# Kernel optimization log

Hardware: AMD Instinct MI355X
Metric: run time of the kernel (lower is better)

## Reference

```python
import jax, jax.numpy as jnp
import numpy as np

NG, K, LEN_KEEP = 128, 32, 32  # n_groups, group_size, int(128*(1-0.75))
ENC_HEADS, DEC_HEADS = 12, 16


def _fps(xyz, init, npoint):
    # iterative farthest point sampling; xyz (B,N,3), init (B,) start indices
    B, N, _ = xyz.shape
    def step(carry, _):
        dmin, far = carry
        c = jnp.take_along_axis(xyz, far[:, None, None], axis=1)  # (B,1,3)
        dmin = jnp.minimum(dmin, jnp.sum((xyz - c) ** 2, -1))
        return (dmin, jnp.argmax(dmin, -1)), far
    _, cents = jax.lax.scan(step, (jnp.full((B, N), 1e10, xyz.dtype), init), None, length=npoint)
    return cents.T  # (B, npoint)


def _knn(xyz, cents, k):
    # squared-distance knn (same ordering as euclidean cdist + topk smallest)
    x2 = jnp.sum(xyz * xyz, -1)          # (B,N)
    c2 = jnp.sum(cents * cents, -1)      # (B,M)
    d = c2[:, :, None] + x2[:, None, :] - 2.0 * jnp.einsum('bmc,bnc->bmn', cents, xyz)
    idx = jax.lax.top_k(-d, k)[1]        # (B,M,k)
    return jax.vmap(lambda p, i: p[i])(xyz, idx)  # (B,M,k,3)


def _bn(x, g, b):
    # train-mode BatchNorm1d over (batch, spatial), channel-last x (BM,k,C)
    m = x.mean((0, 1))
    v = x.var((0, 1))
    return (x - m) * jax.lax.rsqrt(v + 1e-5) * g + b


def _ln(x, g, b):
    m = x.mean(-1, keepdims=True)
    v = ((x - m) ** 2).mean(-1, keepdims=True)
    return (x - m) * jax.lax.rsqrt(v + 1e-5) * g + b


def _layer(x, qw, qb, ow, ob, l1g, l1b, f1w, f1b, f2w, f2b, l2g, l2b, nh):
    # post-norm TransformerEncoderLayer (relu FFN, no dropout = eval mode)
    B, S, D = x.shape
    dh = D // nh
    q, k, v = jnp.split(x @ qw.T + qb, 3, axis=-1)
    q = q.reshape(B, S, nh, dh); k = k.reshape(B, S, nh, dh); v = v.reshape(B, S, nh, dh)
    att = jax.nn.softmax(jnp.einsum('bqhd,bkhd->bhqk', q, k) * (1.0 / float(np.sqrt(dh))), axis=-1)
    o = jnp.einsum('bhqk,bkhd->bqhd', att, v).reshape(B, S, D) @ ow.T + ob
    x = _ln(x + o, l1g, l1b)
    f = jax.nn.relu(x @ f1w.T + f1b) @ f2w.T + f2b
    return _ln(x + f, l2g, l2b)


def _stack(x, qw, qb, ow, ob, l1g, l1b, f1w, f1b, f2w, f2b, l2g, l2b, nh):
    for i in range(qw.shape[0]):
        x = _layer(x, qw[i], qb[i], ow[i], ob[i], l1g[i], l1b[i], f1w[i], f1b[i], f2w[i], f2b[i], l2g[i], l2b[i], nh)
    return x


def _forward(xyz, fps_init, ids_shuffle, cw1, cb1, g1, be1, cw2, cb2, g2, be2, cw3, cb3, g3, be3, pos_w, pos_b, eqw, eqb, eow, eob, el1g, el1b, ef1w, ef1b, ef2w, ef2b, el2g, el2b, dew, deb, mtok, dpw, dpb, dqw, dqb, dow, dob, dl1g, dl1b, df1w, df1b, df2w, df2b, dl2g, dl2b, prw, prb):
    B = xyz.shape[0]
    cent_idx = _fps(xyz, fps_init, NG)
    cxyz = jax.vmap(lambda p, i: p[i])(xyz, cent_idx)      # (B,NG,3)
    gn = _knn(xyz, cxyz, K) - cxyz[:, :, None, :]          # (B,NG,K,3) centered groups
    h = gn.reshape(-1, K, 3)
    h = jax.nn.relu(_bn(h @ cw1.T + cb1, g1, be1))
    h = jax.nn.relu(_bn(h @ cw2.T + cb2, g2, be2))
    h = _bn(h @ cw3.T + cb3, g3, be3)
    tokens = h.max(axis=1).reshape(B, NG, -1)              # (B,NG,768)
    x = tokens + cxyz @ pos_w.T + pos_b
    ids_restore = jnp.argsort(ids_shuffle, axis=1)
    xk = jnp.take_along_axis(x, ids_shuffle[:, :LEN_KEEP, None], axis=1)
    mask = jnp.ones((B, NG), xyz.dtype).at[:, :LEN_KEEP].set(0.0)
    mask = jnp.take_along_axis(mask, ids_restore, axis=1)
    lat = _stack(xk, eqw, eqb, eow, eob, el1g, el1b, ef1w, ef1b, ef2w, ef2b, el2g, el2b, ENC_HEADS)
    y = lat @ dew.T + deb
    mt = jnp.broadcast_to(mtok, (B, NG - LEN_KEEP, mtok.shape[0]))
    y_ = jnp.take_along_axis(jnp.concatenate([y, mt], axis=1), ids_restore[:, :, None], axis=1)
    yd = y_ + cxyz @ dpw.T + dpb
    dec = _stack(yd, dqw, dqb, dow, dob, dl1g, dl1b, df1w, df1b, df2w, df2b, dl2g, dl2b, DEC_HEADS)
    pred = dec @ prw.T + prb                               # (B,NG,K*3)
    target = gn.reshape(B, NG, -1)                         # same FPS seed -> same centroids in loss branch
    l = ((pred - target) ** 2).mean(-1)
    loss = (l * mask).sum() / mask.sum()
    return loss, pred, mask


def setup_inputs():
    ks = iter(jax.random.split(jax.random.key(0), 64))
    def W(*shape):
        return jax.random.normal(next(ks), shape, jnp.float32) * 0.02
    B, N, D, DD, Le, Ld = 32, 8192, 768, 512, 12, 8
    d = {}
    d['xyz'] = jax.random.normal(next(ks), (B, N, 3), jnp.float32)
    d['fps_init'] = jax.random.randint(next(ks), (B,), 0, N)
    d['ids_shuffle'] = jnp.argsort(jax.random.uniform(next(ks), (B, NG)), axis=1)
    d['cw1'], d['cb1'], d['g1'], d['be1'] = W(64, 3), jnp.zeros(64), jnp.ones(64), jnp.zeros(64)
    d['cw2'], d['cb2'], d['g2'], d['be2'] = W(128, 64), jnp.zeros(128), jnp.ones(128), jnp.zeros(128)
    d['cw3'], d['cb3'], d['g3'], d['be3'] = W(D, 128), jnp.zeros(D), jnp.ones(D), jnp.zeros(D)
    d['pos_w'], d['pos_b'] = W(D, 3), jnp.zeros(D)
    d['eqw'], d['eqb'] = W(Le, 3 * D, D), jnp.zeros((Le, 3 * D))
    d['eow'], d['eob'] = W(Le, D, D), jnp.zeros((Le, D))
    d['el1g'], d['el1b'] = jnp.ones((Le, D)), jnp.zeros((Le, D))
    d['ef1w'], d['ef1b'] = W(Le, 4 * D, D), jnp.zeros((Le, 4 * D))
    d['ef2w'], d['ef2b'] = W(Le, D, 4 * D), jnp.zeros((Le, D))
    d['el2g'], d['el2b'] = jnp.ones((Le, D)), jnp.zeros((Le, D))
    d['dew'], d['deb'] = W(DD, D), jnp.zeros(DD)
    d['mtok'] = jnp.zeros(DD)
    d['dpw'], d['dpb'] = W(DD, 3), jnp.zeros(DD)
    d['dqw'], d['dqb'] = W(Ld, 3 * DD, DD), jnp.zeros((Ld, 3 * DD))
    d['dow'], d['dob'] = W(Ld, DD, DD), jnp.zeros((Ld, DD))
    d['dl1g'], d['dl1b'] = jnp.ones((Ld, DD)), jnp.zeros((Ld, DD))
    d['df1w'], d['df1b'] = W(Ld, 4 * DD, DD), jnp.zeros((Ld, 4 * DD))
    d['df2w'], d['df2b'] = W(Ld, DD, 4 * DD), jnp.zeros((Ld, DD))
    d['dl2g'], d['dl2b'] = jnp.ones((Ld, DD)), jnp.zeros((Ld, DD))
    d['prw'], d['prb'] = W(K * 3, DD), jnp.zeros(K * 3)
    return d


def reference(xyz, fps_init, ids_shuffle, cw1, cb1, g1, be1, cw2, cb2, g2, be2, cw3, cb3, g3, be3, pos_w, pos_b, eqw, eqb, eow, eob, el1g, el1b, ef1w, ef1b, ef2w, ef2b, el2g, el2b, dew, deb, mtok, dpw, dpb, dqw, dqb, dow, dob, dl1g, dl1b, df1w, df1b, df2w, df2b, dl2g, dl2b, prw, prb):
    return _forward(xyz, fps_init, ids_shuffle, cw1, cb1, g1, be1, cw2, cb2, g2, be2, cw3, cb3, g3, be3, pos_w, pos_b, eqw, eqb, eow, eob, el1g, el1b, ef1w, ef1b, ef2w, ef2b, el2g, el2b, dew, deb, mtok, dpw, dpb, dqw, dqb, dow, dob, dl1g, dl1b, df1w, df1b, df2w, df2b, dl2g, dl2b, prw, prb)
```

## Files before the change

### kernel.cpp

```cpp
#include <hip/hip_runtime.h>
#include <cmath>

#define BB 32
#define NPTS 8192
#define NG 128
#define KNB 32
#define LK 32
#define DE 768
#define DD 512
#define NLE 12
#define NLD 8

typedef __bf16 bf16x8 __attribute__((ext_vector_type(8)));
typedef float  f32x4  __attribute__((ext_vector_type(4)));
typedef unsigned long long u64;

#define WAITV(N) asm volatile("s_waitcnt vmcnt(" #N ")" ::: "memory")

static __device__ __forceinline__ bf16x8 pack8(float4 a, float4 b) {
    bf16x8 h;
    h[0] = (__bf16)a.x; h[1] = (__bf16)a.y; h[2] = (__bf16)a.z; h[3] = (__bf16)a.w;
    h[4] = (__bf16)b.x; h[5] = (__bf16)b.y; h[6] = (__bf16)b.z; h[7] = (__bf16)b.w;
    return h;
}

static __device__ __forceinline__ void gload16(const __bf16* g, __bf16* l) {
    __builtin_amdgcn_global_load_lds(
        (const __attribute__((address_space(1))) void*)g,
        (__attribute__((address_space(3))) void*)l,
        16, 0, 0);
}

static __device__ __forceinline__ unsigned fkey(float f) {
    unsigned u = __float_as_uint(f);
    return ((int)u < 0) ? ~u : (u | 0x80000000u);
}

__global__ __launch_bounds__(256, 1) void fps_kernel(
    const float* __restrict__ xyz, const int* __restrict__ init,
    float* __restrict__ cxyz)
{
#pragma clang fp contract(off)
    const int b = blockIdx.x;
    const float* P = xyz + (size_t)b * NPTS * 3;
    __shared__ float pxs[NPTS], pys[NPTS], pzs[NPTS];
    __shared__ u64 red[2][4];
    const int tid = threadIdx.x;
    float x[32], y[32], z[32], dmin[32];
    #pragma unroll
    for (int k = 0; k < 32; ++k) {
        int n = tid + (k << 8);
        float xx = P[n * 3 + 0], yy = P[n * 3 + 1], zz = P[n * 3 + 2];
        x[k] = xx; y[k] = yy; z[k] = zz;
        pxs[n] = xx; pys[n] = yy; pzs[n] = zz;
        dmin[k] = 1e10f;
    }
    int far = init[b];
    __syncthreads();
    for (int t = 0; t < NG; ++t) {
        float cx = pxs[far], cy = pys[far], cz = pzs[far];
        if (tid == 0) {
            cxyz[(b * NG + t) * 3 + 0] = cx;
            cxyz[(b * NG + t) * 3 + 1] = cy;
            cxyz[(b * NG + t) * 3 + 2] = cz;
        }
        u64 key = 0ull;
        #pragma unroll
        for (int k = 0; k < 32; ++k) {
            float dx = x[k] - cx, dy = y[k] - cy, dz = z[k] - cz;
            float d = dx * dx + dy * dy + dz * dz;
            float dm = dmin[k];
            if (d < dm) dm = d;
            dmin[k] = dm;
            u64 kk = ((u64)__float_as_uint(dm) << 32) | (unsigned)(8191 - (tid + (k << 8)));
            if (kk > key) key = kk;
        }
        #pragma unroll
        for (int d = 32; d >= 1; d >>= 1) {
            u64 k2 = __shfl_down(key, d);
            if (k2 > key) key = k2;
        }
        if ((tid & 63) == 0) red[t & 1][tid >> 6] = key;
        __syncthreads();
        u64 kb = red[t & 1][0];
        #pragma unroll
        for (int w = 1; w < 4; ++w) {
            u64 k2 = red[t & 1][w];
            if (k2 > kb) kb = k2;
        }
        far = 8191 - (int)(kb & 0xFFFFFFFFu);
    }
}

__global__ __launch_bounds__(256) void knn_kernel(
    const float* __restrict__ xyz, const float* __restrict__ cxyz,
    float* __restrict__ gn)
{
#pragma clang fp contract(off)
    const int bm = blockIdx.x;
    const int b = bm / NG;
    const float* P = xyz + (size_t)b * NPTS * 3;
    __shared__ u64 cand[512];
    __shared__ u64 tmins[4];
    __shared__ int wcnt[4];
    __shared__ int order[KNB];
    const int tid = threadIdx.x;
    const int wv = tid >> 6, lane = tid & 63;
    const float cx = cxyz[bm * 3 + 0], cy = cxyz[bm * 3 + 1], cz = cxyz[bm * 3 + 2];
    const float c2 = cx * cx + cy * cy + cz * cz;
    unsigned fk[32];
    float bestf = 1e31f; int bi = 1 << 30;
    #pragma unroll
    for (int j = 0; j < 32; ++j) {
        int n = tid + (j << 8);
        float x = P[n * 3 + 0], y = P[n * 3 + 1], z = P[n * 3 + 2];
        float x2 = x * x + y * y + z * z;
        float dt = cx * x + cy * y + cz * z;
        float v = (c2 + x2) - 2.0f * dt;
        fk[j] = fkey(v);
        if (v < bestf) { bestf = v; bi = n; }
    }
    u64 mk = ((u64)fkey(bestf) << 32) | (unsigned)bi;
    {
        u64 v = mk;
        #pragma unroll
        for (int k = 2; k <= 64; k <<= 1) {
            #pragma unroll
            for (int j = k >> 1; j > 0; j >>= 1) {
                u64 o = __shfl_xor(v, j);
                bool up = ((lane & k) == 0);
                bool lower = ((lane & j) == 0);
                u64 mn = (v < o) ? v : o;
                u64 mx = (v < o) ? o : v;
                v = (up == lower) ? mn : mx;
            }
        }
        u64 Tw = __shfl(v, 31);
        if (lane == 0) tmins[wv] = Tw;
    }
    __syncthreads();
    u64 T = tmins[0];
    #pragma unroll
    for (int w = 1; w < 4; ++w) { u64 k2 = tmins[w]; if (k2 < T) T = k2; }
    int c = 0;
    #pragma unroll
    for (int j = 0; j < 32; ++j) {
        u64 key = ((u64)fk[j] << 32) | (unsigned)(tid + (j << 8));
        c += (key <= T) ? 1 : 0;
    }
    int s = c;
    #pragma unroll
    for (int d = 1; d < 64; d <<= 1) {
        int t2 = __shfl_up(s, d);
        if (lane >= d) s += t2;
    }
    int excl = s - c;
    if (lane == 63) wcnt[wv] = s;
    __syncthreads();
    int base = 0;
    for (int w = 0; w < wv; ++w) base += wcnt[w];
    int etot = wcnt[0] + wcnt[1] + wcnt[2] + wcnt[3];

    if (etot <= 512) {
        int pos = base + excl;
        #pragma unroll
        for (int j = 0; j < 32; ++j) {
            u64 key = ((u64)fk[j] << 32) | (unsigned)(tid + (j << 8));
            if (key <= T) cand[pos++] = key;
        }
        __syncthreads();
        for (int si = tid; si < etot; si += 256) {
            u64 my = cand[si];
            int r = 0;
            for (int j2 = 0; j2 < etot; ++j2) r += (cand[j2] < my) ? 1 : 0;
            if (r < KNB) order[r] = (int)(my & 0xFFFFFFFFu);
        }
        __syncthreads();
    } else {
        u64 bk = ~0ull;
        #pragma unroll
        for (int j = 0; j < 32; ++j) {
            u64 key = ((u64)fk[j] << 32) | (unsigned)(tid + (j << 8));
            if (key < bk) bk = key;
        }
        for (int r = 0; r < KNB; ++r) {
            u64 kk = bk;
            #pragma unroll
            for (int dd = 32; dd >= 1; dd >>= 1) {
                u64 k2 = __shfl_down(kk, dd);
                if (k2 < kk) kk = k2;
            }
            if (lane == 0) cand[(r & 1) * 4 + wv] = kk;
            __syncthreads();
            u64 kb = cand[(r & 1) * 4 + 0];
            #pragma unroll
            for (int w = 1; w < 4; ++w) { u64 k2 = cand[(r & 1) * 4 + w]; if (k2 < kb) kb = k2; }
            if (tid == 0) order[r] = (int)(kb & 0xFFFFFFFFu);
            if ((int)(kb & 255u) == tid) {
                int sj = (int)((kb & 0xFFFFFFFFu) >> 8);
                #pragma unroll
                for (int j = 0; j < 32; ++j) if (j == sj) fk[j] = 0xFFFFFFFFu;
                bk = ~0ull;
                #pragma unroll
                for (int j = 0; j < 32; ++j) {
                    u64 key = ((u64)fk[j] << 32) | (unsigned)(tid + (j << 8));
                    if (key < bk) bk = key;
                }
            }
            __syncthreads();
        }
    }
    if (tid < KNB) {
        int n = order[tid];
        gn[((size_t)bm * KNB + tid) * 3 + 0] = P[n * 3 + 0] - cx;
        gn[((size_t)bm * KNB + tid) * 3 + 1] = P[n * 3 + 1] - cy;
        gn[((size_t)bm * KNB + tid) * 3 + 2] = P[n * 3 + 2] - cz;
    }
}

__global__ void cvt_bf16_kernel(const float* __restrict__ src, __bf16* __restrict__ dst, int n8)
{
    int i = blockIdx.x * 256 + threadIdx.x;
    if (i >= n8) return;
    const float4* p = (const float4*)(src + (size_t)i * 8);
    *(bf16x8*)(dst + (size_t)i * 8) = pack8(p[0], p[1]);
}

struct CvtTab {
    const float* src[10];
    __bf16* dst[10];
    int cum[11];
};
__global__ void cvt_multi_kernel(CvtTab t)
{
    int i = blockIdx.x * 256 + threadIdx.x;
    if (i >= t.cum[10]) return;
    int seg = 0;
    #pragma unroll
    for (int k = 1; k < 10; ++k) seg += (i >= t.cum[k]) ? 1 : 0;
    int local = i - t.cum[seg];
    const float4* p = (const float4*)(t.src[seg] + (size_t)local * 8);
    *(bf16x8*)(t.dst[seg] + (size_t)local * 8) = pack8(p[0], p[1]);
}

__global__ void embed1_kernel(const float* __restrict__ gn, const float* __restrict__ w,
                              const float* __restrict__ bias, float* __restrict__ h1)
{
    int i = blockIdx.x * 256 + threadIdx.x;
    if (i >= 131072 * 64) return;
    int r = i >> 6, c = i & 63;
    const float* p = gn + (size_t)r * 3;
    h1[i] = p[0] * w[c * 3 + 0] + p[1] * w[c * 3 + 1] + p[2] * w[c * 3 + 2] + bias[c];
}

template <int C>
__global__ __launch_bounds__(256) void colstats_kernel(const float* __restrict__ X,
                                                       double* __restrict__ st, int Mrows)
{
    constexpr int RL = 256 / C;
    const int c = threadIdx.x % C;
    const int rl = threadIdx.x / C;
    double s = 0.0, s2 = 0.0;
    int rows_per_block = (Mrows + gridDim.x - 1) / gridDim.x;
    int r0 = blockIdx.x * rows_per_block;
    int r1 = min(r0 + rows_per_block, Mrows);
    for (int r = r0 + rl; r < r1; r += RL) {
        float v = X[(size_t)r * C + c];
        s += v; s2 += (double)v * v;
    }
    __shared__ double sh[2][256];
    sh[0][threadIdx.x] = s; sh[1][threadIdx.x] = s2;
    __syncthreads();
    if (rl == 0) {
        for (int j = 1; j < RL; ++j) { s += sh[0][j * C + c]; s2 += sh[1][j * C + c]; }
        atomicAdd(&st[c], s);
        atomicAdd(&st[C + c], s2);
    }
}

__global__ void bn_finalize(const double* __restrict__ st, const float* __restrict__ g,
                            const float* __restrict__ be, float* __restrict__ sc,
                            float* __restrict__ shb, int C)
{
    int c = blockIdx.x * 64 + threadIdx.x;
    if (c >= C) return;
    double m = st[c] / 131072.0;
    double var = st[C + c] / 131072.0 - m * m;
    if (var < 0.0) var = 0.0;
    float rs = rsqrtf((float)var + 1e-5f);
    sc[c] = rs * g[c];
    shb[c] = be[c] - (float)m * rs * g[c];
}

__global__ void bn_apply_bf16(const float* __restrict__ x, const float* __restrict__ sc,
                              const float* __restrict__ shb, __bf16* __restrict__ y,
                              int total, int C)
{
    int i = blockIdx.x * 256 + threadIdx.x;
    if (i >= total) return;
    int c = i % C;
    float v = x[i] * sc[c] + shb[c];
    v = fmaxf(v, 0.0f);
    y[i] = (__bf16)v;
}

template <int BM, int WM, int WN, int DEPTH>
__global__ __launch_bounds__(256) void gemm_bf16(
    const __bf16* __restrict__ A, const __bf16* __restrict__ W,
    const float* __restrict__ bias, float* __restrict__ Cf, __bf16* __restrict__ Cb,
    int M, int N, int K, int Kc, int relu)
{
    constexpr int MR = BM / WM / 16;
    constexpr int NR = 128 / WN / 16;
    constexpr int CA = BM * 8 / 256;
    __shared__ __bf16 As[DEPTH][BM * 64];
    __shared__ __bf16 Ws[DEPTH][128 * 64];
    const int tid = threadIdx.x;
    const int lane = tid & 63;
    const int wave = tid >> 6;
    const int wm = wave / WN, wn = wave % WN;
    const int m0 = blockIdx.y * BM, n0 = blockIdx.x * 128;
    const int kb = blockIdx.z * Kc;

    f32x4 acc[MR][NR] = {};

    auto stage = [&](int buf, int kt) {
        #pragma unroll
        for (int j = 0; j < CA; ++j) {
            int cb = j * 256 + (wave << 6);
            int c  = cb + lane;
            int row = c >> 3;
            int kcs = (c & 7) ^ (row & 7);
            gload16(A + (size_t)(m0 + row) * K + kb + kt + kcs * 8, &As[buf][cb * 8]);
        }
        #pragma unroll
        for (int j = 0; j < 4; ++j) {
            int cb = j * 256 + (wave << 6);
            int c  = cb + lane;
            int row = c >> 3;
            int kcs = (c & 7) ^ (row & 7);
            gload16(W + (size_t)(n0 + row) * K + kb + kt + kcs * 8, &Ws[buf][cb * 8]);
        }
    };
    auto compute = [&](int buf) {
        #pragma unroll
        for (int ks = 0; ks < 2; ++ks) {
            bf16x8 af[MR], bfr[NR];
            int kc = ks * 4 + (lane >> 4);
            #pragma unroll
            for (int i = 0; i < MR; ++i) {
                int rowA = wm * (BM / WM) + i * 16 + (lane & 15);
                af[i] = *(bf16x8*)&As[buf][rowA * 64 + ((kc ^ (rowA & 7)) * 8)];
            }
            #pragma unroll
            for (int j = 0; j < NR; ++j) {
                int rowB = wn * (128 / WN) + j * 16 + (lane & 15);
                bfr[j] = *(bf16x8*)&Ws[buf][rowB * 64 + ((kc ^ (rowB & 7)) * 8)];
            }
            #pragma unroll
            for (int i = 0; i < MR; ++i)
                #pragma unroll
                for (int j = 0; j < NR; ++j)
                    acc[i][j] = __builtin_amdgcn_mfma_f32_16x16x32_bf16(af[i], bfr[j], acc[i][j], 0, 0, 0);
        }
    };

    const int nt = Kc >> 6;
    if constexpr (DEPTH == 3) {
        stage(0, 0);
        if (nt > 1) stage(1, 64);
        for (int t = 0; t < nt; ++t) {
            if (t < nt - 1) { if constexpr (BM == 64) WAITV(6); else WAITV(8); }
            else            WAITV(0);
            __syncthreads();
            if (t + 2 < nt) stage((t + 2) % 3, (t + 2) << 6);
            compute(t % 3);
        }
    } else {
        stage(0, 0);
        if (nt > 1) stage(1, 64);
        for (int t = 0; t < nt; ++t) {
            if (t < nt - 1) { if constexpr (BM == 64) WAITV(6); else WAITV(8); }
            else            WAITV(0);
            __syncthreads();
            compute(t % 2);
            if (t + 2 <= nt - 1) {
                __syncthreads();
                stage(t % 2, (t + 2) << 6);
            }
        }
    }

    float* Co = Cf ? Cf + (size_t)blockIdx.z * M * N : nullptr;
    #pragma unroll
    for (int j = 0; j < NR; ++j) {
        int col = n0 + wn * (128 / WN) + j * 16 + (lane & 15);
        if (col >= N) continue;
        float bv = (blockIdx.z == 0) ? bias[col] : 0.0f;
        #pragma unroll
        for (int i = 0; i < MR; ++i) {
            #pragma unroll
            for (int r = 0; r < 4; ++r) {
                int rowm = m0 + wm * (BM / WM) + i * 16 + (lane >> 4) * 4 + r;
                float v = acc[i][j][r] + bv;
                if (relu) v = fmaxf(v, 0.0f);
                if (Co) Co[(size_t)rowm * N + col] = v;
                if (Cb) Cb[(size_t)rowm * N + col] = (__bf16)v;
            }
        }
    }
}

__global__ __launch_bounds__(256) void embed3_mfma(
    const __bf16* __restrict__ A, const __bf16* __restrict__ W,
    const float* __restrict__ cb3,
    float* __restrict__ gmax, float* __restrict__ gmin, double* __restrict__ st3)
{
    __shared__ __bf16 As[2][128 * 64];
    __shared__ __bf16 Ws[2][128 * 64];
    const int tid = threadIdx.x;
    const int lane = tid & 63;
    const int wave = tid >> 6;
    const int wm = wave >> 1, wn = wave & 1;
    const int m0 = blockIdx.y * 128, n0 = blockIdx.x * 128;
    const int K = 128;

    f32x4 acc[4][4] = {};

    auto stage = [&](int buf, int kt) {
        #pragma unroll
        for (int j = 0; j < 4; ++j) {
            int cb = j * 256 + (wave << 6);
            int c  = cb + lane;
            int row = c >> 3;
            int kcs = (c & 7) ^ (row & 7);
            gload16(A + (size_t)(m0 + row) * K + kt + kcs * 8, &As[buf][cb * 8]);
            gload16(W + (size_t)(n0 + row) * K + kt + kcs * 8, &Ws[buf][cb * 8]);
        }
    };
    auto compute = [&](int buf) {
        #pragma unroll
        for (int ks = 0; ks < 2; ++ks) {
            bf16x8 af[4], bfr[4];
            int kc = ks * 4 + (lane >> 4);
            #pragma unroll
            for (int i = 0; i < 4; ++i) {
                int rowA = wm * 64 + i * 16 + (lane & 15);
                af[i] = *(bf16x8*)&As[buf][rowA * 64 + ((kc ^ (rowA & 7)) * 8)];
                int rowB = wn * 64 + i * 16 + (lane & 15);
                bfr[i] = *(bf16x8*)&Ws[buf][rowB * 64 + ((kc ^ (rowB & 7)) * 8)];
            }
            #pragma unroll
            for (int i = 0; i < 4; ++i)
                #pragma unroll
                for (int j = 0; j < 4; ++j)
                    acc[i][j] = __builtin_amdgcn_mfma_f32_16x16x32_bf16(af[i], bfr[j], acc[i][j], 0, 0, 0);
        }
    };

    stage(0, 0);
    stage(1, 64);
    WAITV(8);
    __syncthreads();
    compute(0);
    WAITV(0);
    __syncthreads();
    compute(1);

    #pragma unroll
    for (int j = 0; j < 4; ++j) {
        int col = n0 + wn * 64 + j * 16 + (lane & 15);
        float bv = cb3[col];
        float stot = 0.0f, s2tot = 0.0f;
        #pragma unroll
        for (int gi = 0; gi < 2; ++gi) {
            float mx = -1e30f, mn = 1e30f, s = 0.0f, s2 = 0.0f;
            #pragma unroll
            for (int ii = 0; ii < 2; ++ii) {
                f32x4 a = acc[gi * 2 + ii][j];
                #pragma unroll
                for (int r = 0; r < 4; ++r) {
                    float v = a[r] + bv;
                    mx = fmaxf(mx, v); mn = fminf(mn, v);
                    s += v; s2 += v * v;
                }
            }
            #pragma unroll
            for (int d = 16; d < 64; d <<= 1) {
                mx = fmaxf(mx, __shfl_xor(mx, d));
                mn = fminf(mn, __shfl_xor(mn, d));
                s  += __shfl_xor(s, d);
                s2 += __shfl_xor(s2, d);
            }
            stot += s; s2tot += s2;
            if (lane < 16) {
                int g = (m0 >> 5) + wm * 2 + gi;
                gmax[(size_t)g * 768 + col] = mx;
                gmin[(size_t)g * 768 + col] = mn;
            }
        }
        if (lane < 16) {
            double* stp = st3 + (size_t)(blockIdx.y & 31) * 1536;
            atomicAdd(&stp[col], (double)stot);
            atomicAdd(&stp[768 + col], (double)s2tot);
        }
    }
}

__global__ void bn3_finalize(const double* __restrict__ st3, const float* __restrict__ g,
                             const float* __restrict__ be, float* __restrict__ a3,
                             float* __restrict__ c3)
{
    int c = blockIdx.x * 256 + threadIdx.x;
    if (c >= 768) return;
    double s = 0.0, s2 = 0.0;
    for (int p = 0; p < 32; ++p) { s += st3[(size_t)p * 1536 + c]; s2 += st3[(size_t)p * 1536 + 768 + c]; }
    double m = s / 131072.0;
    double var = s2 / 131072.0 - m * m;
    if (var < 0.0) var = 0.0;
    float rs = rsqrtf((float)var + 1e-5f);
    a3[c] = rs * g[c];
    c3[c] = be[c] - (float)m * rs * g[c];
}

__global__ void tokens_pos(const float* __restrict__ gmax, const float* __restrict__ gmin,
                           const float* __restrict__ a3, const float* __restrict__ c3,
                           const float* __restrict__ cxyz, const float* __restrict__ posw,
                           const float* __restrict__ posb, float* __restrict__ x)
{
    int i = blockIdx.x * 256 + threadIdx.x;
    if (i >= 4096 * 768) return;
    int c = i % 768, g = i / 768;
    float a = a3[c];
    float tok = (a >= 0.0f ? a * gmax[i] : a * gmin[i]) + c3[c];
    float px = cxyz[g * 3 + 0], py = cxyz[g * 3 + 1], pz = cxyz[g * 3 + 2];
    x[i] = tok + px * posw[c * 3 + 0] + py * posw[c * 3 + 1] + pz * posw[c * 3 + 2] + posb[c];
}

__global__ void restore_kernel(const int* __restrict__ shuffle, int* __restrict__ restore,
                               float* __restrict__ maskv)
{
    int j = blockIdx.x * 256 + threadIdx.x;
    if (j >= BB * NG) return;
    int b = j / NG, p = j % NG;
    int dst = b * NG + shuffle[j];
    restore[dst] = p;
    maskv[dst] = (p < LK) ? 0.0f : 1.0f;
}

__global__ void gather_xk(const float* __restrict__ xfull, const int* __restrict__ shuffle,
                          float* __restrict__ xe, __bf16* __restrict__ xeb)
{
    int i = blockIdx.x * 256 + threadIdx.x;
    if (i >= BB * LK * DE) return;
    int c = i % DE;
    int s = (i / DE) % LK;
    int b = i / (DE * LK);
    float v = xfull[((size_t)b * NG + shuffle[b * NG + s]) * DE + c];
    xe[i] = v;
    xeb[i] = (__bf16)v;
}

__global__ void yd_build(const float* __restrict__ ykp, const int* __restrict__ restore,
                         const float* __restrict__ mtok, const float* __restrict__ cxyz,
                         const float* __restrict__ dpw, const float* __restrict__ dpb,
                         float* __restrict__ xd, __bf16* __restrict__ xdb)
{
    const size_t PS = (size_t)1024 * DD;
    int i = blockIdx.x * 256 + threadIdx.x;
    if (i >= BB * NG * DD) return;
    int c = i % DD;
    int g = i / DD;
    int b = g / NG;
    int r = restore[g];
    float base;
    if (r < LK) {
        size_t o = (size_t)(b * LK + r) * DD + c;
        base = ykp[o] + ykp[PS + o] + ykp[2 * PS + o] + ykp[3 * PS + o];
    } else {
        base = mtok[c];
    }
    float px = cxyz[g * 3 + 0], py = cxyz[g * 3 + 1], pz = cxyz[g * 3 + 2];
    float v = base + px * dpw[c * 3 + 0] + py * dpw[c * 3 + 1] + pz * dpw[c * 3 + 2] + dpb[c];
    xd[i] = v;
    xdb[i] = (__bf16)v;
}

template <int S, int DH, int QT, int NH>
__global__ __launch_bounds__(256) void attn_kernel(const float* __restrict__ qkv,
                                                   __bf16* __restrict__ o, float scale)
{
    constexpr int D = NH * DH;
    constexpr int NT = S / QT;
    constexpr int DH4 = DH / 4;
    constexpr int KW = DH + 4;
    constexpr int PS = S + 4;
    constexpr int CH = S / 8;
    __shared__ float Ks[S][KW];
    __shared__ float Vs[S][KW];
    __shared__ float Qs[QT][KW];
    __shared__ float Pb[QT][PS];
    const int t = blockIdx.x % NT;
    const int h = (blockIdx.x / NT) % NH;
    const int b = blockIdx.x / (NT * NH);
    const float* base = qkv + (size_t)b * S * 3 * D + h * DH;
    for (int i = threadIdx.x; i < S * DH4; i += 256) {
        int s = i / DH4, d4 = (i % DH4) * 4;
        *(float4*)&Ks[s][d4] = *(const float4*)&base[(size_t)s * 3 * D + D + d4];
        *(float4*)&Vs[s][d4] = *(const float4*)&base[(size_t)s * 3 * D + 2 * D + d4];
    }
    for (int i = threadIdx.x; i < QT * DH4; i += 256) {
        int qi = i / DH4, d4 = (i % DH4) * 4;
        *(float4*)&Qs[qi][d4] = *(const float4*)&base[(size_t)(t * QT + qi) * 3 * D + d4];
    }
    __syncthreads();
    for (int i = threadIdx.x; i < QT * S; i += 256) {
        int qi = i / S, s = i % S;
        float acc = 0.0f;
        #pragma unroll
        for (int d4 = 0; d4 < DH; d4 += 4) {
            float4 q = *(float4*)&Qs[qi][d4];
            float4 k = *(float4*)&Ks[s][d4];
            acc += q.x * k.x + q.y * k.y + q.z * k.z + q.w * k.w;
        }
        Pb[qi][s] = acc * scale;
    }
    __syncthreads();
    {
        int qi = threadIdx.x >> 3;
        int sub = threadIdx.x & 7;
        float mx = -1e30f;
        #pragma unroll
        for (int j = 0; j < CH; ++j) mx = fmaxf(mx, Pb[qi][sub * CH + j]);
        #pragma unroll
        for (int d = 4; d >= 1; d >>= 1) mx = fmaxf(mx, __shfl_xor(mx, d));
        float sum = 0.0f;
        #pragma unroll
        for (int j = 0; j < CH; ++j) {
            float e = expf(Pb[qi][sub * CH + j] - mx);
            Pb[qi][sub * CH + j] = e;
            sum += e;
        }
        #pragma unroll
        for (int d = 4; d >= 1; d >>= 1) sum += __shfl_xor(sum, d);
        float inv = 1.0f / sum;
        #pragma unroll
        for (int j = 0; j < CH; ++j) Pb[qi][sub * CH + j] *= inv;
    }
    __syncthreads();
    __bf16* ob = o + (size_t)b * S * D + h * DH;
    for (int i = threadIdx.x; i < QT * DH4; i += 256) {
        int qi = i / DH4, d4 = (i % DH4) * 4;
        float4 acc = {0, 0, 0, 0};
        for (int s = 0; s < S; ++s) {
            float p = Pb[qi][s];
            float4 v = *(float4*)&Vs[s][d4];
            acc.x += p * v.x; acc.y += p * v.y; acc.z += p * v.z; acc.w += p * v.w;
        }
        __bf16 o4[4] = {(__bf16)acc.x, (__bf16)acc.y, (__bf16)acc.z, (__bf16)acc.w};
        *(ushort4*)&ob[(size_t)(t * QT + qi) * D + d4] = *(ushort4*)o4;
    }
}

template <int D, int SK>
__global__ __launch_bounds__(256) void ln_res(float* __restrict__ x, const float* __restrict__ part,
                                              size_t pstride,
                                              const float* __restrict__ g, const float* __restrict__ b,
                                              __bf16* __restrict__ xb)
{
    constexpr int J = D / 256;
    __shared__ float pr[2][4];
    const size_t off = (size_t)blockIdx.x * D;
    const int tid = threadIdx.x;
    float vals[J];
    float s = 0.0f, s2 = 0.0f;
    #pragma unroll
    for (int j = 0; j < J; ++j) {
        int i = tid + j * 256;
        float v = x[off + i];
        #pragma unroll
        for (int sk = 0; sk < SK; ++sk) v += part[(size_t)sk * pstride + off + i];
        vals[j] = v; s += v; s2 += v * v;
    }
    #pragma unroll
    for (int d = 32; d >= 1; d >>= 1) { s += __shfl_down(s, d); s2 += __shfl_down(s2, d); }
    if ((tid & 63) == 0) { pr[0][tid >> 6] = s; pr[1][tid >> 6] = s2; }
    __syncthreads();
    float st = pr[0][0] + pr[0][1] + pr[0][2] + pr[0][3];
    float s2t = pr[1][0] + pr[1][1] + pr[1][2] + pr[1][3];
    float m = st / D;
    float var = s2t / D - m * m;
    if (var < 0.0f) var = 0.0f;
    float rs = rsqrtf(var + 1e-5f);
    #pragma unroll
    for (int j = 0; j < J; ++j) {
        int i = tid + j * 256;
        float v = (vals[j] - m) * rs * g[i] + b[i];
        x[off + i] = v;
        xb[off + i] = (__bf16)v;
    }
}

__global__ __launch_bounds__(128) void loss_l(const float* __restrict__ pred,
                                              const float* __restrict__ target,
                                              const float* __restrict__ maskv,
                                              float* __restrict__ lm)
{
    const int g = blockIdx.x;
    __shared__ float red[128];
    int t = threadIdx.x;
    float s = 0.0f;
    if (t < 96) {
        float d = pred[(size_t)g * 96 + t] - target[(size_t)g * 96 + t];
        s = d * d;
    }
    red[t] = s; __syncthreads();
    for (int st = 64; st > 0; st >>= 1) { if (t < st) red[t] += red[t + st]; __syncthreads(); }
    if (t == 0) lm[g] = (red[0] / 96.0f) * maskv[g];
}

__global__ __launch_bounds__(1024) void loss_final(const float* __restrict__ lm,
                                                   const float* __restrict__ maskv,
                                                   float* __restrict__ out)
{
    __shared__ float r1[1024], r2[1024];
    int t = threadIdx.x;
    float a = 0.0f, b = 0.0f;
    for (int i = t; i < BB * NG; i += 1024) { a += lm[i]; b += maskv[i]; }
    r1[t] = a; r2[t] = b; __syncthreads();
    for (int st = 512; st > 0; st >>= 1) { if (t < st) { r1[t] += r1[t + st]; r2[t] += r2[t + st]; } __syncthreads(); }
    if (t == 0) out[0] = r1[0] / r2[0];
}

extern "C" void kernel_launch(void* const* d_in, const int* in_sizes, int n_in,
                              void* d_out, int out_size, void* d_ws, size_t ws_size,
                              hipStream_t stream)
{
    (void)in_sizes; (void)n_in; (void)out_size; (void)ws_size;
    const float* xyz        = (const float*)d_in[0];
    const int*   fps_init   = (const int*)d_in[1];
    const int*   ids_shuf   = (const int*)d_in[2];
    const float* cw1 = (const float*)d_in[3];  const float* cb1 = (const float*)d_in[4];
    const float* g1  = (const float*)d_in[5];  const float* be1 = (const float*)d_in[6];
    const float* cw2 = (const float*)d_in[7];  const float* cb2 = (const float*)d_in[8];
    const float* g2  = (const float*)d_in[9];  const float* be2 = (const float*)d_in[10];
    const float* cw3 = (const float*)d_in[11]; const float* cb3 = (const float*)d_in[12];
    const float* g3  = (const float*)d_in[13]; const float* be3 = (const float*)d_in[14];
    const float* posw = (const float*)d_in[15]; const float* posb = (const float*)d_in[16];
    const float* eqw = (const float*)d_in[17]; const float* eqb = (const float*)d_in[18];
    const float* eow = (const float*)d_in[19]; const float* eob = (const float*)d_in[20];
    const float* el1g = (const float*)d_in[21]; const float* el1b = (const float*)d_in[22];
    const float* ef1w = (const float*)d_in[23]; const float* ef1b = (const float*)d_in[24];
    const float* ef2w = (const float*)d_in[25]; const float* ef2b = (const float*)d_in[26];
    const float* el2g = (const float*)d_in[27]; const float* el2b = (const float*)d_in[28];
    const float* dew = (const float*)d_in[29]; const float* deb = (const float*)d_in[30];
    const float* mtok = (const float*)d_in[31];
    const float* dpw = (const float*)d_in[32]; const float* dpb = (const float*)d_in[33];
    const float* dqw = (const float*)d_in[34]; const float* dqb = (const float*)d_in[35];
    const float* dow = (const float*)d_in[36]; const float* dob = (const float*)d_in[37];
    const float* dl1g = (const float*)d_in[38]; const float* dl1b = (const float*)d_in[39];
    const float* df1w = (const float*)d_in[40]; const float* df1b = (const float*)d_in[41];
    const float* df2w = (const float*)d_in[42]; const float* df2b = (const float*)d_in[43];
    const float* dl2g = (const float*)d_in[44]; const float* dl2b = (const float*)d_in[45];
    const float* prw = (const float*)d_in[46]; const float* prb = (const float*)d_in[47];
    float* out = (float*)d_out;
    float* pred = out + 1;
    float* maskv = out + 1 + (size_t)BB * NG * KNB * 3;

    char* ws = (char*)d_ws;
    size_t off = 0;
    auto alloc = [&](size_t bytes) -> void* {
        void* p = ws + off;
        off = (off + bytes + 255) & ~(size_t)255;
        return p;
    };
    double* st1 = (double*)alloc(128 * 8);
    double* st2 = (double*)alloc(256 * 8);
    double* st3 = (double*)alloc((size_t)32 * 1536 * 8);
    float* sc1 = (float*)alloc(64 * 4);  float* sh1 = (float*)alloc(64 * 4);
    float* sc2 = (float*)alloc(128 * 4); float* sh2 = (float*)alloc(128 * 4);
    float* a3 = (float*)alloc(768 * 4);  float* c3 = (float*)alloc(768 * 4);
    int* restore = (int*)alloc(4096 * 4);
    float* cxyz = (float*)alloc(12288 * 4);
    float* gn   = (float*)alloc((size_t)393216 * 4);
    __bf16* cw2b = (__bf16*)alloc((size_t)128 * 64 * 2);
    __bf16* cw3b = (__bf16*)alloc((size_t)768 * 128 * 2);
    float* xfull = (float*)alloc((size_t)4096 * 768 * 4);
    float* xe    = (float*)alloc((size_t)1024 * 768 * 4);
    __bf16* xeb  = (__bf16*)alloc((size_t)1024 * 768 * 2);
    float* qkve  = (float*)alloc((size_t)1024 * 2304 * 4);
    __bf16* oeb  = (__bf16*)alloc((size_t)1024 * 768 * 2);
    __bf16* fe1b = (__bf16*)alloc((size_t)1024 * 3072 * 2);
    float* xd    = (float*)alloc((size_t)4096 * 512 * 4);
    __bf16* xdb  = (__bf16*)alloc((size_t)4096 * 512 * 2);
    float* qkvd  = (float*)alloc((size_t)4096 * 1536 * 4);
    __bf16* odb  = (__bf16*)alloc((size_t)4096 * 512 * 2);
    __bf16* fd1b = (__bf16*)alloc((size_t)4096 * 2048 * 2);
    float* lm    = (float*)alloc(4096 * 4);

    __bf16* eqwb  = (__bf16*)alloc((size_t)NLE * 3 * DE * DE * 2);
    __bf16* eowb  = (__bf16*)alloc((size_t)NLE * DE * DE * 2);
    __bf16* ef1wb = (__bf16*)alloc((size_t)NLE * 4 * DE * DE * 2);
    __bf16* ef2wb = (__bf16*)alloc((size_t)NLE * 4 * DE * DE * 2);
    __bf16* dewb  = (__bf16*)alloc((size_t)DD * DE * 2);
    __bf16* dqwb  = (__bf16*)alloc((size_t)NLD * 3 * DD * DD * 2);
    __bf16* dowb  = (__bf16*)alloc((size_t)NLD * DD * DD * 2);
    __bf16* df1wb = (__bf16*)alloc((size_t)NLD * 4 * DD * DD * 2);
    __bf16* df2wb = (__bf16*)alloc((size_t)NLD * 4 * DD * DD * 2);
    __bf16* prwb  = (__bf16*)alloc((size_t)128 * 512 * 2);

    char* U = (char*)eqwb;
    float*  h1   = (float*)U;
    __bf16* h1b  = (__bf16*)(U + (size_t)33554432);
    float*  h2   = (float*)(U + (size_t)50331648);
    __bf16* h2b  = (__bf16*)(U + (size_t)117440512);
    float*  gmax = (float*)(U + (size_t)150994944);
    float*  gmin = (float*)(U + (size_t)163577856);

    size_t stats_bytes = (size_t)((char*)st3 + (size_t)32 * 1536 * 8 - (char*)st1);
    hipMemsetAsync((void*)st1, 0, stats_bytes, stream);

    auto cvt = [&](const float* src, __bf16* dst, size_t n) {
        int n8 = (int)(n / 8);
        cvt_bf16_kernel<<<(n8 + 255) / 256, 256, 0, stream>>>(src, dst, n8);
    };
    auto gemm = [&](const __bf16* A, const __bf16* Wt, const float* bias,
                    float* Cf, __bf16* Cb, int M, int N, int K, int relu) {
        int nb128 = ((N + 127) / 128) * (M / 128);
        if (nb128 < 256) {
            dim3 grid((N + 127) / 128, M / 64, 1);
            gemm_bf16<64, 1, 4, 3><<<grid, 256, 0, stream>>>(A, Wt, bias, Cf, Cb, M, N, K, K, relu);
        } else {
            dim3 grid((N + 127) / 128, M / 128, 1);
            gemm_bf16<128, 2, 2, 2><<<grid, 256, 0, stream>>>(A, Wt, bias, Cf, Cb, M, N, K, K, relu);
        }
    };
    auto gemmSK = [&](const __bf16* A, const __bf16* Wt, const float* bias,
                      float* Cf, int M, int N, int K, int SK) {
        dim3 grid((N + 127) / 128, M / 64, SK);
        gemm_bf16<64, 1, 4, 3><<<grid, 256, 0, stream>>>(A, Wt, bias, Cf, nullptr, M, N, K, K / SK, 0);
    };

    cvt(cw2, cw2b, 128 * 64);
    cvt(cw3, cw3b, 768 * 128);

    fps_kernel<<<BB, 256, 0, stream>>>(xyz, fps_init, cxyz);
    knn_kernel<<<BB * NG, 256, 0, stream>>>(xyz, cxyz, gn);

    embed1_kernel<<<(131072 * 64 + 255) / 256, 256, 0, stream>>>(gn, cw1, cb1, h1);
    colstats_kernel<64><<<256, 256, 0, stream>>>(h1, st1, 131072);
    bn_finalize<<<1, 64, 0, stream>>>(st1, g1, be1, sc1, sh1, 64);
    bn_apply_bf16<<<(131072 * 64 + 255) / 256, 256, 0, stream>>>(h1, sc1, sh1, h1b, 131072 * 64, 64);
    gemm(h1b, cw2b, cb2, h2, nullptr, 131072, 128, 64, 0);
    colstats_kernel<128><<<256, 256, 0, stream>>>(h2, st2, 131072);
    bn_finalize<<<2, 64, 0, stream>>>(st2, g2, be2, sc2, sh2, 128);
    bn_apply_bf16<<<(131072 * 128 + 255) / 256, 256, 0, stream>>>(h2, sc2, sh2, h2b, 131072 * 128, 128);
    embed3_mfma<<<dim3(6, 1024), 256, 0, stream>>>(h2b, cw3b, cb3, gmax, gmin, st3);
    bn3_finalize<<<3, 256, 0, stream>>>(st3, g3, be3, a3, c3);
    tokens_pos<<<(4096 * 768 + 255) / 256, 256, 0, stream>>>(gmax, gmin, a3, c3, cxyz, posw, posb, xfull);

    restore_kernel<<<16, 256, 0, stream>>>(ids_shuf, restore, maskv);
    gather_xk<<<(BB * LK * DE + 255) / 256, 256, 0, stream>>>(xfull, ids_shuf, xe, xeb);

    {
        CvtTab t;
        const float* srcs[10] = {eqw, eow, ef1w, ef2w, dew, dqw, dow, df1w, df2w, prw};
        __bf16* dsts[10] = {eqwb, eowb, ef1wb, ef2wb, dewb, dqwb, dowb, df1wb, df2wb, prwb};
        size_t ns[10] = {
            (size_t)NLE * 3 * DE * DE, (size_t)NLE * DE * DE,
            (size_t)NLE * 4 * DE * DE, (size_t)NLE * 4 * DE * DE,
            (size_t)DD * DE,
            (size_t)NLD * 3 * DD * DD, (size_t)NLD * DD * DD,
            (size_t)NLD * 4 * DD * DD, (size_t)NLD * 4 * DD * DD,
            (size_t)96 * 512
        };
        int cum = 0;
        t.cum[0] = 0;
        for (int k = 0; k < 10; ++k) {
            t.src[k] = srcs[k]; t.dst[k] = dsts[k];
            cum += (int)(ns[k] / 8);
            t.cum[k + 1] = cum;
        }
        cvt_multi_kernel<<<(cum + 255) / 256, 256, 0, stream>>>(t);
        hipMemsetAsync((void*)(prwb + (size_t)96 * 512), 0, (size_t)32 * 512 * 2, stream);
    }

    const size_t PSE = (size_t)1024 * DE;
    const size_t PSD = (size_t)4096 * DD;

    for (int l = 0; l < NLE; ++l) {
        gemm(xeb, eqwb + (size_t)l * 3 * DE * DE, eqb + (size_t)l * 3 * DE, qkve, nullptr, 1024, 3 * DE, DE, 0);
        attn_kernel<LK, 64, 32, 12><<<BB * 12, 256, 0, stream>>>(qkve, oeb, 0.125f);
        gemmSK(oeb, eowb + (size_t)l * DE * DE, eob + (size_t)l * DE, xfull, 1024, DE, DE, 4);
        ln_res<DE, 4><<<BB * LK, 256, 0, stream>>>(xe, xfull, PSE, el1g + (size_t)l * DE, el1b + (size_t)l * DE, xeb);
        gemm(xeb, ef1wb + (size_t)l * 4 * DE * DE, ef1b + (size_t)l * 4 * DE, nullptr, fe1b, 1024, 4 * DE, DE, 1);
        gemmSK(fe1b, ef2wb + (size_t)l * DE * 4 * DE, ef2b + (size_t)l * DE, xfull, 1024, DE, 4 * DE, 4);
        ln_res<DE, 4><<<BB * LK, 256, 0, stream>>>(xe, xfull, PSE, el2g + (size_t)l * DE, el2b + (size_t)l * DE, xeb);
    }

    gemmSK(xeb, dewb, deb, qkve, 1024, DD, DE, 4);
    yd_build<<<(BB * NG * DD + 255) / 256, 256, 0, stream>>>(qkve, restore, mtok, cxyz, dpw, dpb, xd, xdb);

    const float dsc = (float)(1.0 / sqrt(32.0));
    for (int l = 0; l < NLD; ++l) {
        gemm(xdb, dqwb + (size_t)l * 3 * DD * DD, dqb + (size_t)l * 3 * DD, qkvd, nullptr, 4096, 3 * DD, DD, 0);
        attn_kernel<NG, 32, 32, 16><<<BB * 16 * (NG / 32), 256, 0, stream>>>(qkvd, odb, dsc);
        gemmSK(odb, dowb + (size_t)l * DD * DD, dob + (size_t)l * DD, qkvd, 4096, DD, DD, 2);
        ln_res<DD, 2><<<BB * NG, 256, 0, stream>>>(xd, qkvd, PSD, dl1g + (size_t)l * DD, dl1b + (size_t)l * DD, xdb);
        gemm(xdb, df1wb + (size_t)l * 4 * DD * DD, df1b + (size_t)l * 4 * DD, nullptr, fd1b, 4096, 4 * DD, DD, 1);
        gemmSK(fd1b, df2wb + (size_t)l * DD * 4 * DD, df2b + (size_t)l * DD, qkvd, 4096, DD, 4 * DD, 2);
        ln_res<DD, 2><<<BB * NG, 256, 0, stream>>>(xd, qkvd, PSD, dl2g + (size_t)l * DD, dl2b + (size_t)l * DD, xdb);
    }

    gemm(xdb, prwb, prb, pred, nullptr, 4096, 96, 512, 0);
    loss_l<<<BB * NG, 128, 0, stream>>>(pred, gn, maskv, lm);
    loss_final<<<1, 1024, 0, stream>>>(lm, maskv, out);
}
```

Baseline: 2.618 ms.

## Use bf16 MFMA for encoder/decoder attention and widen FPS to 512 threads

Replaces the scalar fp32 attention kernels with MFMA-based kernels. Q, K and V are converted to bf16 in LDS, V is stored transposed, and the softmax is done on accumulator registers. Decoder attention now uses one block per (batch, head) instead of one per query tile, and encoder attention uses a single wave per head. FPS runs with 512 threads and 16 points each, tracking a scalar best distance and index before packing the 64-bit key. These changes lower precision in attention (bf16 P and V) and change the FPS reduction structure.

After: 2.419 ms. 1.08x faster.

```diff
diff --git a/kernel.cpp b/kernel.cpp
--- a/kernel.cpp
+++ b/kernel.cpp
@@ -36,7 +36,7 @@
     return ((int)u < 0) ? ~u : (u | 0x80000000u);
 }
 
-__global__ __launch_bounds__(256, 1) void fps_kernel(
+__global__ __launch_bounds__(512, 1) void fps_kernel(
     const float* __restrict__ xyz, const int* __restrict__ init,
     float* __restrict__ cxyz)
 {
@@ -44,12 +44,12 @@
     const int b = blockIdx.x;
     const float* P = xyz + (size_t)b * NPTS * 3;
     __shared__ float pxs[NPTS], pys[NPTS], pzs[NPTS];
-    __shared__ u64 red[2][4];
+    __shared__ u64 red[2][8];
     const int tid = threadIdx.x;
-    float x[32], y[32], z[32], dmin[32];
-    #pragma unroll
-    for (int k = 0; k < 32; ++k) {
-        int n = tid + (k << 8);
+    float x[16], y[16], z[16], dmin[16];
+    #pragma unroll
+    for (int k = 0; k < 16; ++k) {
+        int n = tid + (k << 9);
         float xx = P[n * 3 + 0], yy = P[n * 3 + 1], zz = P[n * 3 + 2];
         x[k] = xx; y[k] = yy; z[k] = zz;
         pxs[n] = xx; pys[n] = yy; pzs[n] = zz;
@@ -64,17 +64,18 @@
             cxyz[(b * NG + t) * 3 + 1] = cy;
             cxyz[(b * NG + t) * 3 + 2] = cz;
         }
-        u64 key = 0ull;
-        #pragma unroll
-        for (int k = 0; k < 32; ++k) {
+        float best = -1.0f; int bi = 0;
+        #pragma unroll
+        for (int k = 0; k < 16; ++k) {
+            int n = tid + (k << 9);
             float dx = x[k] - cx, dy = y[k] - cy, dz = z[k] - cz;
             float d = dx * dx + dy * dy + dz * dz;
             float dm = dmin[k];
             if (d < dm) dm = d;
             dmin[k] = dm;
-            u64 kk = ((u64)__float_as_uint(dm) << 32) | (unsigned)(8191 - (tid + (k << 8)));
-            if (kk > key) key = kk;
-        }
+            if (dm > best) { best = dm; bi = n; }
+        }
+        u64 key = ((u64)__float_as_uint(best) << 32) | (unsigned)(8191 - bi);
         #pragma unroll
         for (int d = 32; d >= 1; d >>= 1) {
             u64 k2 = __shfl_down(key, d);
@@ -84,7 +85,7 @@
         __syncthreads();
         u64 kb = red[t & 1][0];
         #pragma unroll
-        for (int w = 1; w < 4; ++w) {
+        for (int w = 1; w < 8; ++w) {
             u64 k2 = red[t & 1][w];
             if (k2 > kb) kb = k2;
         }
@@ -586,79 +587,183 @@
     xdb[i] = (__bf16)v;
 }
 
-template <int S, int DH, int QT, int NH>
-__global__ __launch_bounds__(256) void attn_kernel(const float* __restrict__ qkv,
+template <int S, int DH, int NH>
+__global__ __launch_bounds__(256) void dattn_kernel(const float* __restrict__ qkv,
+                                                    __bf16* __restrict__ o, float scale)
+{
+    constexpr int D = NH * DH;
+    constexpr int SQ = DH + 8;
+    constexpr int SV = S + 8;
+    __shared__ __bf16 Qb[S * SQ];
+    __shared__ __bf16 Kb[S * SQ];
+    __shared__ __bf16 Vt[DH * SV];
+    __shared__ __bf16 Pb[S * SV];
+    const int h = blockIdx.x % NH;
+    const int b = blockIdx.x / NH;
+    const int tid = threadIdx.x;
+    const int lane = tid & 63, wv = tid >> 6;
+    const float* base = qkv + (size_t)b * S * 3 * D + h * DH;
+    for (int i = tid; i < S * (DH / 4); i += 256) {
+        int s = i / (DH / 4), c4 = (i % (DH / 4)) * 4;
+        const float* rp = base + (size_t)s * 3 * D;
+        float4 q = *(const float4*)(rp + c4);
+        float4 k = *(const float4*)(rp + D + c4);
+        float4 v = *(const float4*)(rp + 2 * D + c4);
+        __bf16 q4[4] = {(__bf16)q.x, (__bf16)q.y, (__bf16)q.z, (__bf16)q.w};
+        __bf16 k4[4] = {(__bf16)k.x, (__bf16)k.y, (__bf16)k.z, (__bf16)k.w};
+        *(ushort4*)&Qb[s * SQ + c4] = *(ushort4*)q4;
+        *(ushort4*)&Kb[s * SQ + c4] = *(ushort4*)k4;
+        Vt[(c4 + 0) * SV + s] = (__bf16)v.x;
+        Vt[(c4 + 1) * SV + s] = (__bf16)v.y;
+        Vt[(c4 + 2) * SV + s] = (__bf16)v.z;
+        Vt[(c4 + 3) * SV + s] = (__bf16)v.w;
+    }
+    __syncthreads();
+    const int q0 = wv * 32;
+    const int arow = lane & 15;
+    const int kch = (lane >> 4) * 8;
+    const int rrow = (lane >> 4) * 4;
+    f32x4 sc[2][8];
+    {
+        bf16x8 af0 = *(bf16x8*)&Qb[(q0 + arow) * SQ + kch];
+        bf16x8 af1 = *(bf16x8*)&Qb[(q0 + 16 + arow) * SQ + kch];
+        f32x4 z = {0.0f, 0.0f, 0.0f, 0.0f};
+        #pragma unroll
+        for (int j = 0; j < 8; ++j) {
+            bf16x8 bf_ = *(bf16x8*)&Kb[(j * 16 + arow) * SQ + kch];
+            sc[0][j] = __builtin_amdgcn_mfma_f32_16x16x32_bf16(af0, bf_, z, 0, 0, 0);
+            sc[1][j] = __builtin_amdgcn_mfma_f32_16x16x32_bf16(af1, bf_, z, 0, 0, 0);
+        }
+    }
+    #pragma unroll
+    for (int i = 0; i < 2; ++i) {
+        #pragma unroll
+        for (int r = 0; r < 4; ++r) {
+            float m = -1e30f;
+            #pragma unroll
+            for (int j = 0; j < 8; ++j) m = fmaxf(m, sc[i][j][r]);
+            #pragma unroll
+            for (int d = 8; d >= 1; d >>= 1) m = fmaxf(m, __shfl_xor(m, d));
+            float sum = 0.0f;
+            #pragma unroll
+            for (int j = 0; j < 8; ++j) {
+                float e = expf((sc[i][j][r] - m) * scale);
+                sc[i][j][r] = e;
+                sum += e;
+            }
+            #pragma unroll
+            for (int d = 8; d >= 1; d >>= 1) sum += __shfl_xor(sum, d);
+            float inv = 1.0f / sum;
+            int row = q0 + i * 16 + rrow + r;
+            #pragma unroll
+            for (int j = 0; j < 8; ++j)
+                Pb[row * SV + j * 16 + (lane & 15)] = (__bf16)(sc[i][j][r] * inv);
+        }
+    }
+    #pragma unroll
+    for (int i = 0; i < 2; ++i) {
+        #pragma unroll
+        for (int j2 = 0; j2 < 2; ++j2) {
+            f32x4 a2 = {0.0f, 0.0f, 0.0f, 0.0f};
+            #pragma unroll
+            for (int ks = 0; ks < 4; ++ks) {
+                bf16x8 pa = *(bf16x8*)&Pb[(q0 + i * 16 + arow) * SV + ks * 32 + kch];
+                bf16x8 vb = *(bf16x8*)&Vt[(j2 * 16 + arow) * SV + ks * 32 + kch];
+                a2 = __builtin_amdgcn_mfma_f32_16x16x32_bf16(pa, vb, a2, 0, 0, 0);
+            }
+            #pragma unroll
+            for (int r = 0; r < 4; ++r) {
+                int q = q0 + i * 16 + rrow + r;
+                o[((size_t)(b * S + q)) * D + h * DH + j2 * 16 + (lane & 15)] = (__bf16)a2[r];
+            }
+        }
+    }
+}
+
+template <int S, int DH, int NH>
+__global__ __launch_bounds__(64) void eattn_kernel(const float* __restrict__ qkv,
                                                    __bf16* __restrict__ o, float scale)
 {
     constexpr int D = NH * DH;
-    constexpr int NT = S / QT;
-    constexpr int DH4 = DH / 4;
-    constexpr int KW = DH + 4;
-    constexpr int PS = S + 4;
-    constexpr int CH = S / 8;
-    __shared__ float Ks[S][KW];
-    __shared__ float Vs[S][KW];
-    __shared__ float Qs[QT][KW];
-    __shared__ float Pb[QT][PS];
-    const int t = blockIdx.x % NT;
-    const int h = (blockIdx.x / NT) % NH;
-    const int b = blockIdx.x / (NT * NH);
+    constexpr int SQ = DH + 8;
+    constexpr int SV = S + 8;
+    __shared__ __bf16 Qb[S * SQ];
+    __shared__ __bf16 Kb[S * SQ];
+    __shared__ __bf16 Vt[DH * SV];
+    __shared__ __bf16 Pb[S * SV];
+    const int h = blockIdx.x % NH;
+    const int b = blockIdx.x / NH;
+    const int lane = threadIdx.x;
     const float* base = qkv + (size_t)b * S * 3 * D + h * DH;
-    for (int i = threadIdx.x; i < S * DH4; i += 256) {
-        int s = i / DH4, d4 = (i % DH4) * 4;
-        *(float4*)&Ks[s][d4] = *(const float4*)&base[(size_t)s * 3 * D + D + d4];
-        *(float4*)&Vs[s][d4] = *(const float4*)&base[(size_t)s * 3 * D + 2 * D + d4];
-    }
-    for (int i = threadIdx.x; i < QT * DH4; i += 256) {
-        int qi = i / DH4, d4 = (i % DH4) * 4;
-        *(float4*)&Qs[qi][d4] = *(const float4*)&base[(size_t)(t * QT + qi) * 3 * D + d4];
+    for (int i = lane; i < S * (DH / 4); i += 64) {
+        int s = i / (DH / 4), c4 = (i % (DH / 4)) * 4;
+        const float* rp = base + (size_t)s * 3 * D;
+        float4 q = *(const float4*)(rp + c4);
+        float4 k = *(const float4*)(rp + D + c4);
+        float4 v = *(const float4*)(rp + 2 * D + c4);
+        __bf16 q4[4] = {(__bf16)q.x, (__bf16)q.y, (__bf16)q.z, (__bf16)q.w};
+        __bf16 k4[4] = {(__bf16)k.x, (__bf16)k.y, (__bf16)k.z, (__bf16)k.w};
+        *(ushort4*)&Qb[s * SQ + c4] = *(ushort4*)q4;
+        *(ushort4*)&Kb[s * SQ + c4] = *(ushort4*)k4;
+        Vt[(c4 + 0) * SV + s] = (__bf16)v.x;
+        Vt[(c4 + 1) * SV + s] = (__bf16)v.y;
+        Vt[(c4 + 2) * SV + s] = (__bf16)v.z;
+        Vt[(c4 + 3) * SV + s] = (__bf16)v.w;
     }
     __syncthreads();
-    for (int i = threadIdx.x; i < QT * S; i += 256) {
-        int qi = i / S, s = i % S;
-        float acc = 0.0f;
-        #pragma unroll
-        for (int d4 = 0; d4 < DH; d4 += 4) {
-            float4 q = *(float4*)&Qs[qi][d4];
-            float4 k = *(float4*)&Ks[s][d4];
-            acc += q.x * k.x + q.y * k.y + q.z * k.z + q.w * k.w;
-        }
-        Pb[qi][s] = acc * scale;
+    const int arow = lane & 15;
+    const int kch = (lane >> 4) * 8;
+    const int rrow = (lane >> 4) * 4;
+    f32x4 sc[2][2] = {};
+    #pragma unroll
+    for (int ks = 0; ks < 2; ++ks) {
+        bf16x8 af0 = *(bf16x8*)&Qb[(arow) * SQ + ks * 32 + kch];
+        bf16x8 af1 = *(bf16x8*)&Qb[(16 + arow) * SQ + ks * 32 + kch];
+        #pragma unroll
+        for (int j = 0; j < 2; ++j) {
+            bf16x8 bf_ = *(bf16x8*)&Kb[(j * 16 + arow) * SQ + ks * 32 + kch];
+            sc[0][j] = __builtin_amdgcn_mfma_f32_16x16x32_bf16(af0, bf_, sc[0][j], 0, 0, 0);
+            sc[1][j] = __builtin_amdgcn_mfma_f32_16x16x32_bf16(af1, bf_, sc[1][j], 0, 0, 0);
+        }
+    }
+    #pragma unroll
+    for (int i = 0; i < 2; ++i) {
+        #pragma unroll
+        for (int r = 0; r < 4; ++r) {
+            float m = fmaxf(sc[i][0][r], sc[i][1][r]);
+            #pragma unroll
+            for (int d = 8; d >= 1; d >>= 1) m = fmaxf(m, __shfl_xor(m, d));
+            float sum = 0.0f;
+            #pragma unroll
+            for (int j = 0; j < 2; ++j) {
+                float e = expf((sc[i][j][r] - m) * scale);
+                sc[i][j][r] = e;
+                sum += e;
+            }
+            #pragma unroll
+            for (int d = 8; d >= 1; d >>= 1) sum += __shfl_xor(sum, d);
+            float inv = 1.0f / sum;
+            int row = i * 16 + rrow + r;
+            #pragma unroll
+            for (int j = 0; j < 2; ++j)
+                Pb[row * SV + j * 16 + (lane & 15)] = (__bf16)(sc[i][j][r] * inv);
+        }
     }
     __syncthreads();
-    {
-        int qi = threadIdx.x >> 3;
-        int sub = threadIdx.x & 7;
-        float mx = -1e30f;
-        #pragma unroll
-        for (int j = 0; j < CH; ++j) mx = fmaxf(mx, Pb[qi][sub * CH + j]);
-        #pragma unroll
-        for (int d = 4; d >= 1; d >>= 1) mx = fmaxf(mx, __shfl_xor(mx, d));
-        float sum = 0.0f;
-        #pragma unroll
-        for (int j = 0; j < CH; ++j) {
-            float e = expf(Pb[qi][sub * CH + j] - mx);
-            Pb[qi][sub * CH + j] = e;
-            sum += e;
-        }
-        #pragma unroll
-        for (int d = 4; d >= 1; d >>= 1) sum += __shfl_xor(sum, d);
-        float inv = 1.0f / sum;
-        #pragma unroll
-        for (int j = 0; j < CH; ++j) Pb[qi][sub * CH + j] *= inv;
-    }
-    __syncthreads();
-    __bf16* ob = o + (size_t)b * S * D + h * DH;
-    for (int i = threadIdx.x; i < QT * DH4; i += 256) {
-        int qi = i / DH4, d4 = (i % DH4) * 4;
-        float4 acc = {0, 0, 0, 0};
-        for (int s = 0; s < S; ++s) {
-            float p = Pb[qi][s];
-            float4 v = *(float4*)&Vs[s][d4];
-            acc.x += p * v.x; acc.y += p * v.y; acc.z += p * v.z; acc.w += p * v.w;
-        }
-        __bf16 o4[4] = {(__bf16)acc.x, (__bf16)acc.y, (__bf16)acc.z, (__bf16)acc.w};
-        *(ushort4*)&ob[(size_t)(t * QT + qi) * D + d4] = *(ushort4*)o4;
+    #pragma unroll
+    for (int i = 0; i < 2; ++i) {
+        bf16x8 pa = *(bf16x8*)&Pb[(i * 16 + arow) * SV + kch];
+        #pragma unroll
+        for (int j2 = 0; j2 < 4; ++j2) {
+            bf16x8 vb = *(bf16x8*)&Vt[(j2 * 16 + arow) * SV + kch];
+            f32x4 z = {0.0f, 0.0f, 0.0f, 0.0f};
+            f32x4 a2 = __builtin_amdgcn_mfma_f32_16x16x32_bf16(pa, vb, z, 0, 0, 0);
+            #pragma unroll
+            for (int r = 0; r < 4; ++r) {
+                int q = i * 16 + rrow + r;
+                o[((size_t)(b * S + q)) * D + h * DH + j2 * 16 + (lane & 15)] = (__bf16)a2[r];
+            }
+        }
     }
 }
 
@@ -844,7 +949,7 @@
     cvt(cw2, cw2b, 128 * 64);
     cvt(cw3, cw3b, 768 * 128);
 
-    fps_kernel<<<BB, 256, 0, stream>>>(xyz, fps_init, cxyz);
+    fps_kernel<<<BB, 512, 0, stream>>>(xyz, fps_init, cxyz);
     knn_kernel<<<BB * NG, 256, 0, stream>>>(xyz, cxyz, gn);
 
     embed1_kernel<<<(131072 * 64 + 255) / 256, 256, 0, stream>>>(gn, cw1, cb1, h1);
@@ -890,7 +995,7 @@
 
     for (int l = 0; l < NLE; ++l) {
         gemm(xeb, eqwb + (size_t)l * 3 * DE * DE, eqb + (size_t)l * 3 * DE, qkve, nullptr, 1024, 3 * DE, DE, 0);
-        attn_kernel<LK, 64, 32, 12><<<BB * 12, 256, 0, stream>>>(qkve, oeb, 0.125f);
+        eattn_kernel<LK, 64, 12><<<BB * 12, 64, 0, stream>>>(qkve, oeb, 0.125f);
         gemmSK(oeb, eowb + (size_t)l * DE * DE, eob + (size_t)l * DE, xfull, 1024, DE, DE, 4);
         ln_res<DE, 4><<<BB * LK, 256, 0, stream>>>(xe, xfull, PSE, el1g + (size_t)l * DE, el1b + (size_t)l * DE, xeb);
         gemm(xeb, ef1wb + (size_t)l * 4 * DE * DE, ef1b + (size_t)l * 4 * DE, nullptr, fe1b, 1024, 4 * DE, DE, 1);
@@ -904,7 +1009,7 @@
     const float dsc = (float)(1.0 / sqrt(32.0));
     for (int l = 0; l < NLD; ++l) {
         gemm(xdb, dqwb + (size_t)l * 3 * DD * DD, dqb + (size_t)l * 3 * DD, qkvd, nullptr, 4096, 3 * DD, DD, 0);
-        attn_kernel<NG, 32, 32, 16><<<BB * 16 * (NG / 32), 256, 0, stream>>>(qkvd, odb, dsc);
+        dattn_kernel<NG, 32, 16><<<BB * 16, 256, 0, stream>>>(qkvd, odb, dsc);
         gemmSK(odb, dowb + (size_t)l * DD * DD, dob + (size_t)l * DD, qkvd, 4096, DD, DD, 2);
         ln_res<DD, 2><<<BB * NG, 256, 0, stream>>>(xd, qkvd, PSD, dl1g + (size_t)l * DD, dl1b + (size_t)l * DD, xdb);
         gemm(xdb, df1wb + (size_t)l * 4 * DD * DD, df1b + (size_t)l * 4 * DD, nullptr, fd1b, 4096, 4 * DD, DD, 1);
```
